# Optimization experiments

Measured on AMD Instinct MI355X. Metric: run time of the kernel, lower is better.

The kernel has to match this reference:

```python
import jax, jax.numpy as jnp
import numpy as np

N_NODES = 100000
N_EDGES = 3200000
D_IN = 128
HEADS = 8
F_OUT = 64


def setup_inputs() -> dict:
    key = jax.random.key(0)
    k1, k2, k3, k4, k5, k6 = jax.random.split(key, 6)
    node_features = jax.random.normal(k1, (N_NODES, D_IN), dtype=jnp.float32)
    linear_proj = jax.random.normal(k2, (D_IN, HEADS * F_OUT), dtype=jnp.float32) * (1.0 / np.sqrt(D_IN))
    scoring_fn_source = jax.random.normal(k3, (1, HEADS, F_OUT), dtype=jnp.float32) * 0.1
    scoring_fn_target = jax.random.normal(k4, (1, HEADS, F_OUT), dtype=jnp.float32) * 0.1
    edge_index = jax.random.randint(k5, (2, N_EDGES), 0, N_NODES, dtype=jnp.int64)
    return {
        'node_features': node_features,
        'linear_proj': linear_proj,
        'scoring_fn_source': scoring_fn_source,
        'scoring_fn_target': scoring_fn_target,
        'edge_index': edge_index,
    }


def reference(node_features, linear_proj, scoring_fn_source, scoring_fn_target, edge_index):
    # node_features: [N, D_in]; edge_index: [2, E] (row 0 = src, row 1 = trg)
    N = node_features.shape[0]
    H, F = scoring_fn_source.shape[1], scoring_fn_source.shape[2]

    # linear projection: [N, H, F]
    proj = (node_features @ linear_proj).reshape(N, H, F)

    # per-node attention scores: [N, H]
    scores_source = jnp.sum(proj * scoring_fn_source, axis=-1)
    scores_target = jnp.sum(proj * scoring_fn_target, axis=-1)

    src, trg = edge_index[0], edge_index[1]
    # lift to edges + LeakyReLU: [E, H]
    scores_per_edge = jax.nn.leaky_relu(scores_source[src] + scores_target[trg],
                                        negative_slope=0.2)

    # neighborhood-aware softmax over edges sharing the same target node
    seg_max = jax.ops.segment_max(scores_per_edge, trg, num_segments=N)   # [N, H]
    exp_scores = jnp.exp(scores_per_edge - seg_max[trg])                  # [E, H]
    seg_sum = jax.ops.segment_sum(exp_scores, trg, num_segments=N)        # [N, H]
    attentions_per_edge = exp_scores / (seg_sum[trg] + 1e-16)             # [E, H]
    return attentions_per_edge
```

## Files before the change

### kernel.cpp

```cpp
#include <hip/hip_runtime.h>
#include <hip/hip_fp16.h>

#define D_IN   128
#define HEADS  8
#define FOUT   64
#define NOUT   16
#define NPB    128
#define NB_MAX 1024
#define CHUNK  4096
#define NBLK_MAX 1024
#define TPN    8
#define SROWS  64
#define SPAD   129

typedef unsigned __attribute__((ext_vector_type(2))) uint2v;
typedef float    __attribute__((ext_vector_type(4))) float4v;

__device__ __forceinline__ unsigned pack2(float a, float b) {
    union { __half2 h; unsigned u; } c;
    c.h = __floats2half2_rn(a, b);
    return c.u;
}
__device__ __forceinline__ float2 up2(unsigned u) {
    union { unsigned x; __half2 h; } c;
    c.x = u;
    return __half22float2(c.h);
}

__device__ __forceinline__ unsigned ntl_u(const unsigned* p) {
    return __builtin_nontemporal_load(p);
}
__device__ __forceinline__ uint2v ntl_u2(const unsigned* p) {
    return __builtin_nontemporal_load((const uint2v*)p);
}
__device__ __forceinline__ float4v ntl_f4(const float* p) {
    return __builtin_nontemporal_load((const float4v*)p);
}
__device__ __forceinline__ void nts_f4(float* p, float4v v) {
    __builtin_nontemporal_store(v, (float4v*)p);
}

__global__ void k_detect(const unsigned int* __restrict__ idx_w, int nwords,
                         unsigned int* __restrict__ flag) {
    unsigned int local = 0;
    int stride = gridDim.x * blockDim.x;
    for (int i = blockIdx.x * blockDim.x + threadIdx.x; 2 * i + 1 < nwords; i += stride)
        local |= idx_w[2 * i + 1];
    if (__any(local != 0) && (threadIdx.x & 63) == 0)
        atomicOr(flag, 1u);
}

__device__ __forceinline__ void load_edge(const unsigned int* idx, int e, int E,
                                          bool is64, unsigned int& s, unsigned int& t) {
    if (is64) {
        uint2v a = ntl_u2(idx + 2 * (size_t)e);
        uint2v b = ntl_u2(idx + 2 * ((size_t)E + e));
        s = a.x; t = b.x;
    } else {
        s = ntl_u(idx + e);
        t = ntl_u(idx + (size_t)E + e);
    }
}

__device__ __forceinline__ unsigned int load_trg(const unsigned int* idx, int e, int E,
                                                 bool is64) {
    if (is64) { uint2v b = ntl_u2(idx + 2 * ((size_t)E + e)); return b.x; }
    return ntl_u(idx + (size_t)E + e);
}

__global__ void k_fold_w(const float* __restrict__ W,
                         const float* __restrict__ a_src,
                         const float* __restrict__ a_trg,
                         float* __restrict__ Wc,
                         unsigned int* __restrict__ flag) {
    int t = blockIdx.x * blockDim.x + threadIdx.x;
    if (t == 0) *flag = 0u;
    if (t >= D_IN * HEADS) return;
    int d = t >> 3, h = t & 7;
    const float* wrow = W + d * (HEADS * FOUT) + h * FOUT;
    float s1 = 0.f, s2 = 0.f;
    #pragma unroll 4
    for (int f = 0; f < FOUT; ++f) {
        float w = wrow[f];
        s1 += w * a_src[h * FOUT + f];
        s2 += w * a_trg[h * FOUT + f];
    }
    Wc[h * D_IN + d]           = s1;
    Wc[(HEADS + h) * D_IN + d] = s2;
}

__global__ void k_scores_t(const float* __restrict__ x,
                           const float* __restrict__ Wc,
                           float* __restrict__ ssrc_f,
                           float* __restrict__ strg_f,
                           __half* __restrict__ ssrc_h, int N) {
    __shared__ float xt[SROWS * SPAD];
    int node0 = blockIdx.x * SROWS;
    int tid   = threadIdx.x;
    int nrows = min(SROWS, N - node0);

    for (int i = tid; i < nrows * 32; i += 256) {
        int r = i >> 5, c = (i & 31) * 4;
        float4v v = ntl_f4(x + (size_t)(node0 + r) * D_IN + c);
        float* dst = &xt[r * SPAD + c];
        dst[0] = v.x; dst[1] = v.y; dst[2] = v.z; dst[3] = v.w;
    }
    __syncthreads();

    int r  = tid & 63;
    int og = tid >> 6;
    if (r >= nrows) return;
    int n = node0 + r;

    const float* w = Wc + og * 4 * D_IN;
    float a0 = 0.f, a1 = 0.f, a2 = 0.f, a3 = 0.f;
    const float* xr = &xt[r * SPAD];
    #pragma unroll 8
    for (int d = 0; d < D_IN; ++d) {
        float xv = xr[d];
        a0 += xv * w[d];
        a1 += xv * w[D_IN + d];
        a2 += xv * w[2 * D_IN + d];
        a3 += xv * w[3 * D_IN + d];
    }

    float4 res = make_float4(a0, a1, a2, a3);
    if (og < 2) *(float4*)(ssrc_f + (size_t)n * HEADS + og * 4)       = res;
    else        *(float4*)(strg_f + (size_t)n * HEADS + (og - 2) * 4) = res;
    if (og < 2) {
        uint2 hp;
        hp.x = pack2(a0, a1);
        hp.y = pack2(a2, a3);
        *(uint2*)(ssrc_h + (size_t)n * HEADS + og * 4) = hp;
    }
}

__global__ void k_hist(const unsigned int* __restrict__ idx, int E,
                       const unsigned int* __restrict__ flag,
                       int* __restrict__ histB, int NB, int NBLK) {
    __shared__ int h[NB_MAX];
    for (int i = threadIdx.x; i < NB; i += blockDim.x) h[i] = 0;
    __syncthreads();
    bool is64 = (*flag == 0u);
    int base = blockIdx.x * CHUNK;
    int lim  = min(base + CHUNK, E);
    for (int e = base + threadIdx.x; e < lim; e += blockDim.x) {
        unsigned int t = load_trg(idx, e, E, is64);
        atomicAdd(&h[t >> 7], 1);
    }
    __syncthreads();
    for (int i = threadIdx.x; i < NB; i += blockDim.x)
        histB[(size_t)i * NBLK + blockIdx.x] = h[i];
}

__global__ void k_scan_blocks(const int* __restrict__ histB,
                              int* __restrict__ histA, int NB, int NBLK,
                              int* __restrict__ binTotal) {
    int b = blockIdx.x;
    __shared__ int v[NBLK_MAX];
    int tid = threadIdx.x;
    v[tid] = (tid < NBLK) ? histB[(size_t)b * NBLK + tid] : 0;
    __syncthreads();
    for (int off = 1; off < NBLK_MAX; off <<= 1) {
        int t = (tid >= off) ? v[tid - off] : 0;
        __syncthreads();
        v[tid] += t;
        __syncthreads();
    }
    if (tid < NBLK)
        histA[(size_t)tid * NB + b] = tid ? v[tid - 1] : 0;
    if (tid == 0)
        binTotal[b] = v[NBLK_MAX - 1];
}

__global__ void k_scan_bins(const int* __restrict__ binTotal, int NB,
                            int* __restrict__ binBase) {
    __shared__ int v[NB_MAX];
    int tid = threadIdx.x;
    v[tid] = (tid < NB) ? binTotal[tid] : 0;
    __syncthreads();
    for (int off = 1; off < NB_MAX; off <<= 1) {
        int t = (tid >= off) ? v[tid - off] : 0;
        __syncthreads();
        v[tid] += t;
        __syncthreads();
    }
    if (tid < NB)
        binBase[tid] = tid ? v[tid - 1] : 0;
}

__global__ void k_scatter(const unsigned int* __restrict__ idx, int E,
                          const unsigned int* __restrict__ flag,
                          const int* __restrict__ histA, int NB,
                          const int* __restrict__ binBase,
                          unsigned int* __restrict__ binned) {
    __shared__ int cnt[NB_MAX];
    for (int i = threadIdx.x; i < NB; i += blockDim.x)
        cnt[i] = binBase[i] + histA[(size_t)blockIdx.x * NB + i];
    __syncthreads();
    bool is64 = (*flag == 0u);
    int base = blockIdx.x * CHUNK;
    int lim  = min(base + CHUNK, E);
    for (int e = base + threadIdx.x; e < lim; e += blockDim.x) {
        unsigned int s, t;
        load_edge(idx, e, E, is64, s, t);
        int pos = atomicAdd(&cnt[t >> 7], 1);
        binned[pos] = s | ((t & 127u) << 20);
    }
}

__global__ void k_sort2(const unsigned int* __restrict__ binned,
                        const int* __restrict__ binBase,
                        const int* __restrict__ binTotal,
                        unsigned int* __restrict__ sortedSrc,
                        int* __restrict__ rowPtr, int N, int NB) {
    __shared__ int cnt[NPB];
    __shared__ int scn[NPB];
    int b = blockIdx.x;
    int node0 = b << 7;
    int start = binBase[b], total = binTotal[b];
    int i = threadIdx.x;

    if (i < NPB) cnt[i] = 0;
    __syncthreads();
    for (int e = i; e < total; e += blockDim.x)
        atomicAdd(&cnt[binned[start + e] >> 20], 1);
    __syncthreads();

    if (i < NPB) scn[i] = cnt[i];
    __syncthreads();
    for (int off = 1; off < NPB; off <<= 1) {
        int t = (i < NPB && i >= off) ? scn[i - off] : 0;
        __syncthreads();
        if (i < NPB) scn[i] += t;
        __syncthreads();
    }
    if (i < NPB) {
        int excl = scn[i] - cnt[i];
        cnt[i] = excl;
        int n = node0 + i;
        if (n < N) rowPtr[n] = start + excl;
    }
    if (b == NB - 1 && i == 0) rowPtr[N] = start + total;
    __syncthreads();

    for (int e = i; e < total; e += blockDim.x) {
        unsigned int v = binned[start + e];
        int pos = atomicAdd(&cnt[v >> 20], 1);
        sortedSrc[start + pos] = v & 0xFFFFFu;
    }
}

__global__ void k_nodesum(const unsigned int* __restrict__ sortedSrc,
                          const int* __restrict__ rowPtr,
                          const __half* __restrict__ ssrc_h,
                          const float* __restrict__ strg_f,
                          __half* __restrict__ combo, int N) {
    int gt = blockIdx.x * blockDim.x + threadIdx.x;
    int n  = gt >> 3;
    int k  = gt & (TPN - 1);
    if (n >= N) return;

    int r0 = rowPtr[n], r1 = rowPtr[n + 1];
    const float4* tp = (const float4*)(strg_f + (size_t)n * HEADS);
    float4 ta = tp[0], tb = tp[1];
    float st[8] = { ta.x, ta.y, ta.z, ta.w, tb.x, tb.y, tb.z, tb.w };
    float acc[8] = { 0, 0, 0, 0, 0, 0, 0, 0 };

    for (int e = r0 + k; e < r1; e += TPN) {
        unsigned int s = sortedSrc[e];
        uint4 sv = *(const uint4*)(ssrc_h + (size_t)s * HEADS);
        float2 f01 = up2(sv.x), f23 = up2(sv.y), f45 = up2(sv.z), f67 = up2(sv.w);
        float vs[8] = { f01.x, f01.y, f23.x, f23.y, f45.x, f45.y, f67.x, f67.y };
        #pragma unroll
        for (int h = 0; h < HEADS; ++h) {
            float sc = vs[h] + st[h];
            sc = sc > 0.f ? sc : 0.2f * sc;
            acc[h] += expf(sc);
        }
    }
    #pragma unroll
    for (int h = 0; h < HEADS; ++h) {
        acc[h] += __shfl_xor(acc[h], 1, 64);
        acc[h] += __shfl_xor(acc[h], 2, 64);
        acc[h] += __shfl_xor(acc[h], 4, 64);
    }
    if (k == 0) {
        float rs[8];
        #pragma unroll
        for (int h = 0; h < HEADS; ++h) rs[h] = 1.0f / (acc[h] + 1e-16f);
        uint4 c0, c1;
        c0.x = pack2(st[0], st[1]);  c0.y = pack2(st[2], st[3]);
        c0.z = pack2(st[4], st[5]);  c0.w = pack2(st[6], st[7]);
        c1.x = pack2(rs[0], rs[1]);  c1.y = pack2(rs[2], rs[3]);
        c1.z = pack2(rs[4], rs[5]);  c1.w = pack2(rs[6], rs[7]);
        uint4* cp = (uint4*)(combo + (size_t)n * 16);
        cp[0] = c0;
        cp[1] = c1;
    }
}

__global__ void k_edge_out_c(const unsigned int* __restrict__ idx, int E,
                             const __half* __restrict__ ssrc_h,
                             const __half* __restrict__ combo,
                             const unsigned int* __restrict__ flag,
                             float* __restrict__ out) {
    int e = blockIdx.x * blockDim.x + threadIdx.x;
    if (e >= E) return;
    bool is64 = (*flag == 0u);
    unsigned int s, t;
    load_edge(idx, e, E, is64, s, t);

    uint4 sv = *(const uint4*)(ssrc_h + (size_t)s * HEADS);
    const uint4* cp = (const uint4*)(combo + (size_t)t * 16);
    uint4 c0 = cp[0], c1 = cp[1];

    float2 s01 = up2(sv.x), s23 = up2(sv.y), s45 = up2(sv.z), s67 = up2(sv.w);
    float2 t01 = up2(c0.x), t23 = up2(c0.y), t45 = up2(c0.z), t67 = up2(c0.w);
    float2 r01 = up2(c1.x), r23 = up2(c1.y), r45 = up2(c1.z), r67 = up2(c1.w);

    float ss[8] = { s01.x, s01.y, s23.x, s23.y, s45.x, s45.y, s67.x, s67.y };
    float st[8] = { t01.x, t01.y, t23.x, t23.y, t45.x, t45.y, t67.x, t67.y };
    float rs[8] = { r01.x, r01.y, r23.x, r23.y, r45.x, r45.y, r67.x, r67.y };

    float o[8];
    #pragma unroll
    for (int h = 0; h < HEADS; ++h) {
        float sc = ss[h] + st[h];
        sc = sc > 0.f ? sc : 0.2f * sc;
        o[h] = expf(sc) * rs[h];
    }
    float4v o0 = { o[0], o[1], o[2], o[3] };
    float4v o1 = { o[4], o[5], o[6], o[7] };
    nts_f4(out + (size_t)e * HEADS,     o0);
    nts_f4(out + (size_t)e * HEADS + 4, o1);
}

__device__ __forceinline__ void edge_scores(const float* ssrc, const float* strg,
                                            unsigned int s, unsigned int t, float* ex) {
    const float4* sp = (const float4*)(ssrc + (size_t)s * HEADS);
    const float4* tp = (const float4*)(strg + (size_t)t * HEADS);
    float4 sa = sp[0], sb = sp[1], ta = tp[0], tb = tp[1];
    float v[8] = { sa.x + ta.x, sa.y + ta.y, sa.z + ta.z, sa.w + ta.w,
                   sb.x + tb.x, sb.y + tb.y, sb.z + tb.z, sb.w + tb.w };
    #pragma unroll
    for (int h = 0; h < HEADS; ++h) {
        float sc = v[h];
        sc = sc > 0.f ? sc : 0.2f * sc;
        ex[h] = expf(sc);
    }
}

__global__ void k_edge_sum(const unsigned int* __restrict__ idx, int E,
                           const float* __restrict__ ssrc,
                           const float* __restrict__ strg,
                           float* __restrict__ sums,
                           const unsigned int* __restrict__ flag) {
    int e = blockIdx.x * blockDim.x + threadIdx.x;
    if (e >= E) return;
    bool is64 = (*flag == 0u);
    unsigned int s, t;
    load_edge(idx, e, E, is64, s, t);
    float ex[8];
    edge_scores(ssrc, strg, s, t, ex);
    float* dst = sums + (size_t)t * HEADS;
    #pragma unroll
    for (int h = 0; h < HEADS; ++h)
        atomicAdd(dst + h, ex[h]);
}

__global__ void k_edge_out(const unsigned int* __restrict__ idx, int E,
                           const float* __restrict__ ssrc,
                           const float* __restrict__ strg,
                           const float* __restrict__ sums,
                           const unsigned int* __restrict__ flag,
                           float* __restrict__ out) {
    int e = blockIdx.x * blockDim.x + threadIdx.x;
    if (e >= E) return;
    bool is64 = (*flag == 0u);
    unsigned int s, t;
    load_edge(idx, e, E, is64, s, t);
    float ex[8];
    edge_scores(ssrc, strg, s, t, ex);
    const float4* sm = (const float4*)(sums + (size_t)t * HEADS);
    float4 m0 = sm[0], m1 = sm[1];
    float4 o0, o1;
    o0.x = ex[0] / (m0.x + 1e-16f);  o0.y = ex[1] / (m0.y + 1e-16f);
    o0.z = ex[2] / (m0.z + 1e-16f);  o0.w = ex[3] / (m0.w + 1e-16f);
    o1.x = ex[4] / (m1.x + 1e-16f);  o1.y = ex[5] / (m1.y + 1e-16f);
    o1.z = ex[6] / (m1.z + 1e-16f);  o1.w = ex[7] / (m1.w + 1e-16f);
    float4* op = (float4*)(out + (size_t)e * HEADS);
    op[0] = o0;
    op[1] = o1;
}

extern "C" void kernel_launch(void* const* d_in, const int* in_sizes, int n_in,
                              void* d_out, int out_size, void* d_ws, size_t ws_size,
                              hipStream_t stream) {
    const float*        x     = (const float*)d_in[0];
    const float*        W     = (const float*)d_in[1];
    const float*        a_src = (const float*)d_in[2];
    const float*        a_trg = (const float*)d_in[3];
    const unsigned int* idx   = (const unsigned int*)d_in[4];

    const int N  = in_sizes[0] / D_IN;
    const int E  = in_sizes[4] / 2;
    const int NH = N * HEADS;
    const int NB   = (N + NPB - 1) / NPB;
    const int NBLK = (E + CHUNK - 1) / CHUNK;

    float* out = (float*)d_out;

    char*  ws  = (char*)d_ws;
    size_t off = 0;
    auto alloc = [&](size_t bytes) { size_t o = off; off = (off + bytes + 255) & ~(size_t)255; return o; };
    size_t NHb = (size_t)NH * sizeof(float);
    float*        sums     = (float*)(ws + alloc(NHb));
    unsigned int* flag     = (unsigned int*)(ws + alloc(4));
    float*        ssrc_f   = (float*)(ws + alloc(NHb));
    float*        strg_f   = (float*)(ws + alloc(NHb));
    __half*       ssrc_h   = (__half*)(ws + alloc((size_t)NH * sizeof(__half)));
    __half*       combo    = (__half*)(ws + alloc((size_t)N * 16 * sizeof(__half)));
    float*        Wc       = (float*)(ws + alloc(NOUT * D_IN * sizeof(float)));
    int*          histA    = (int*)(ws + alloc((size_t)NBLK * NB * sizeof(int)));
    int*          histB    = (int*)(ws + alloc((size_t)NB * NBLK * sizeof(int)));
    int*          binTotal = (int*)(ws + alloc((size_t)NB * sizeof(int)));
    int*          binBase  = (int*)(ws + alloc((size_t)NB * sizeof(int)));
    unsigned int* binned   = (unsigned int*)(ws + alloc((size_t)E * sizeof(unsigned int)));
    unsigned int* sortedS  = (unsigned int*)(ws + alloc((size_t)E * sizeof(unsigned int)));
    int*          rowPtr   = (int*)(ws + alloc((size_t)(N + 1) * sizeof(int)));

    const bool fast = (off <= ws_size) && (NB <= NB_MAX) && (NBLK <= NBLK_MAX)
                      && (N < (1 << 20));

    if (!fast)
        hipMemsetAsync(sums, 0, NHb, stream);

    k_fold_w <<<(D_IN * HEADS + 255) / 256, 256, 0, stream>>>(W, a_src, a_trg, Wc, flag);

    int dwords = in_sizes[4];
    if (dwords > (1 << 20)) dwords = 1 << 20;
    k_detect <<<128, 256, 0, stream>>>(idx, dwords, flag);

    k_scores_t <<<(N + SROWS - 1) / SROWS, 256, 0, stream>>>(x, Wc, ssrc_f, strg_f,
                                                             ssrc_h, N);

    int eblocks = (E + 255) / 256;
    if (fast) {
        k_hist        <<<NBLK, 512, 0, stream>>>(idx, E, flag, histB, NB, NBLK);
        k_scan_blocks <<<NB, NBLK_MAX, 0, stream>>>(histB, histA, NB, NBLK, binTotal);
        k_scan_bins   <<<1, NB_MAX, 0, stream>>>(binTotal, NB, binBase);
        k_scatter     <<<NBLK, 512, 0, stream>>>(idx, E, flag, histA, NB, binBase, binned);
        k_sort2       <<<NB, 512, 0, stream>>>(binned, binBase, binTotal, sortedS,
                                               rowPtr, N, NB);
        k_nodesum     <<<(N * TPN + 511) / 512, 512, 0, stream>>>(sortedS, rowPtr,
                                                                  ssrc_h, strg_f,
                                                                  combo, N);
        k_edge_out_c  <<<eblocks, 256, 0, stream>>>(idx, E, ssrc_h, combo, flag, out);
    } else {
        k_edge_sum <<<eblocks, 256, 0, stream>>>(idx, E, ssrc_f, strg_f, sums, flag);
        k_edge_out <<<eblocks, 256, 0, stream>>>(idx, E, ssrc_f, strg_f, sums, flag, out);
    }
}
```

Measured before the change: 261.4 us.

## Fuse sort with node sums, merge scans, fold detect into score kernel

Fuses the per-bin counting sort with the per-node exp-sum reduction so the sorted sources are consumed in the same block, which removes the rowPtr array and a separate launch. Bin totals are now accumulated with atomics in the histogram kernel, so the two scan kernels merge into one launch. Index-width detection moves into the first blocks of the score kernel. Bin size grows to 512 nodes and chunk size to 8192 edges, which cuts launch count and the size of the histogram scan, at the cost of fewer, larger sort blocks with more shared-memory atomic contention.

```diff
diff --git a/kernel.cpp b/kernel.cpp
--- a/kernel.cpp
+++ b/kernel.cpp
@@ -5,13 +5,15 @@
 #define HEADS  8
 #define FOUT   64
 #define NOUT   16
-#define NPB    128
+#define NPB    512
+#define NPB_SH 9
 #define NB_MAX 1024
-#define CHUNK  4096
+#define CHUNK  8192
 #define NBLK_MAX 1024
 #define TPN    8
 #define SROWS  64
 #define SPAD   129
+#define DET_BLOCKS 128
 
 typedef unsigned __attribute__((ext_vector_type(2))) uint2v;
 typedef float    __attribute__((ext_vector_type(4))) float4v;
@@ -38,16 +40,6 @@
 }
 __device__ __forceinline__ void nts_f4(float* p, float4v v) {
     __builtin_nontemporal_store(v, (float4v*)p);
-}
-
-__global__ void k_detect(const unsigned int* __restrict__ idx_w, int nwords,
-                         unsigned int* __restrict__ flag) {
-    unsigned int local = 0;
-    int stride = gridDim.x * blockDim.x;
-    for (int i = blockIdx.x * blockDim.x + threadIdx.x; 2 * i + 1 < nwords; i += stride)
-        local |= idx_w[2 * i + 1];
-    if (__any(local != 0) && (threadIdx.x & 63) == 0)
-        atomicOr(flag, 1u);
 }
 
 __device__ __forceinline__ void load_edge(const unsigned int* idx, int e, int E,
@@ -72,9 +64,11 @@
                          const float* __restrict__ a_src,
                          const float* __restrict__ a_trg,
                          float* __restrict__ Wc,
-                         unsigned int* __restrict__ flag) {
+                         unsigned int* __restrict__ flag,
+                         int* __restrict__ binTotal, int NB) {
     int t = blockIdx.x * blockDim.x + threadIdx.x;
     if (t == 0) *flag = 0u;
+    if (t < NB) binTotal[t] = 0;
     if (t >= D_IN * HEADS) return;
     int d = t >> 3, h = t & 7;
     const float* wrow = W + d * (HEADS * FOUT) + h * FOUT;
@@ -93,7 +87,18 @@
                            const float* __restrict__ Wc,
                            float* __restrict__ ssrc_f,
                            float* __restrict__ strg_f,
-                           __half* __restrict__ ssrc_h, int N) {
+                           __half* __restrict__ ssrc_h, int N,
+                           const unsigned int* __restrict__ idx_w, int dwords,
+                           unsigned int* __restrict__ flag) {
+    if (blockIdx.x < DET_BLOCKS) {
+        unsigned int local = 0;
+        int stride = DET_BLOCKS * 256;
+        for (int i = blockIdx.x * 256 + threadIdx.x; 2 * i + 1 < dwords; i += stride)
+            local |= idx_w[2 * i + 1];
+        if (__any(local != 0) && (threadIdx.x & 63) == 0)
+            atomicOr(flag, 1u);
+    }
+
     __shared__ float xt[SROWS * SPAD];
     int node0 = blockIdx.x * SROWS;
     int tid   = threadIdx.x;
@@ -137,7 +142,8 @@
 
 __global__ void k_hist(const unsigned int* __restrict__ idx, int E,
                        const unsigned int* __restrict__ flag,
-                       int* __restrict__ histB, int NB, int NBLK) {
+                       int* __restrict__ histB, int NB, int NBLK,
+                       int* __restrict__ binTotal) {
     __shared__ int h[NB_MAX];
     for (int i = threadIdx.x; i < NB; i += blockDim.x) h[i] = 0;
     __syncthreads();
@@ -146,47 +152,46 @@
     int lim  = min(base + CHUNK, E);
     for (int e = base + threadIdx.x; e < lim; e += blockDim.x) {
         unsigned int t = load_trg(idx, e, E, is64);
-        atomicAdd(&h[t >> 7], 1);
-    }
-    __syncthreads();
-    for (int i = threadIdx.x; i < NB; i += blockDim.x)
+        atomicAdd(&h[t >> NPB_SH], 1);
+    }
+    __syncthreads();
+    for (int i = threadIdx.x; i < NB; i += blockDim.x) {
         histB[(size_t)i * NBLK + blockIdx.x] = h[i];
-}
-
-__global__ void k_scan_blocks(const int* __restrict__ histB,
-                              int* __restrict__ histA, int NB, int NBLK,
-                              int* __restrict__ binTotal) {
+        if (h[i]) atomicAdd(&binTotal[i], h[i]);
+    }
+}
+
+__global__ void k_scan(const int* __restrict__ histB,
+                       int* __restrict__ histA, int NB, int NBLK,
+                       const int* __restrict__ binTotal,
+                       int* __restrict__ binBase) {
     int b = blockIdx.x;
-    __shared__ int v[NBLK_MAX];
     int tid = threadIdx.x;
-    v[tid] = (tid < NBLK) ? histB[(size_t)b * NBLK + tid] : 0;
-    __syncthreads();
-    for (int off = 1; off < NBLK_MAX; off <<= 1) {
-        int t = (tid >= off) ? v[tid - off] : 0;
+    if (b < NB) {
+        __shared__ int v[NBLK_MAX];
+        v[tid] = (tid < NBLK) ? histB[(size_t)b * NBLK + tid] : 0;
         __syncthreads();
-        v[tid] += t;
+        for (int off = 1; off < NBLK_MAX; off <<= 1) {
+            int t = (tid >= off) ? v[tid - off] : 0;
+            __syncthreads();
+            v[tid] += t;
+            __syncthreads();
+        }
+        if (tid < NBLK)
+            histA[(size_t)tid * NB + b] = tid ? v[tid - 1] : 0;
+    } else {
+        __shared__ int v[NB_MAX];
+        v[tid] = (tid < NB) ? binTotal[tid] : 0;
         __syncthreads();
-    }
-    if (tid < NBLK)
-        histA[(size_t)tid * NB + b] = tid ? v[tid - 1] : 0;
-    if (tid == 0)
-        binTotal[b] = v[NBLK_MAX - 1];
-}
-
-__global__ void k_scan_bins(const int* __restrict__ binTotal, int NB,
-                            int* __restrict__ binBase) {
-    __shared__ int v[NB_MAX];
-    int tid = threadIdx.x;
-    v[tid] = (tid < NB) ? binTotal[tid] : 0;
-    __syncthreads();
-    for (int off = 1; off < NB_MAX; off <<= 1) {
-        int t = (tid >= off) ? v[tid - off] : 0;
-        __syncthreads();
-        v[tid] += t;
-        __syncthreads();
-    }
-    if (tid < NB)
-        binBase[tid] = tid ? v[tid - 1] : 0;
+        for (int off = 1; off < NB_MAX; off <<= 1) {
+            int t = (tid >= off) ? v[tid - off] : 0;
+            __syncthreads();
+            v[tid] += t;
+            __syncthreads();
+        }
+        if (tid < NB)
+            binBase[tid] = tid ? v[tid - 1] : 0;
+    }
 }
 
 __global__ void k_scatter(const unsigned int* __restrict__ idx, int E,
@@ -204,99 +209,96 @@
     for (int e = base + threadIdx.x; e < lim; e += blockDim.x) {
         unsigned int s, t;
         load_edge(idx, e, E, is64, s, t);
-        int pos = atomicAdd(&cnt[t >> 7], 1);
-        binned[pos] = s | ((t & 127u) << 20);
-    }
-}
-
-__global__ void k_sort2(const unsigned int* __restrict__ binned,
-                        const int* __restrict__ binBase,
-                        const int* __restrict__ binTotal,
-                        unsigned int* __restrict__ sortedSrc,
-                        int* __restrict__ rowPtr, int N, int NB) {
+        int pos = atomicAdd(&cnt[t >> NPB_SH], 1);
+        binned[pos] = s | ((t & (NPB - 1u)) << 20);
+    }
+}
+
+__global__ void k_sortsum(const unsigned int* __restrict__ binned,
+                          const int* __restrict__ binBase,
+                          const int* __restrict__ binTotal,
+                          const __half* __restrict__ ssrc_h,
+                          const float* __restrict__ strg_f,
+                          unsigned int* __restrict__ sortedSrc,
+                          __half* __restrict__ combo, int N, int NB) {
     __shared__ int cnt[NPB];
     __shared__ int scn[NPB];
+    __shared__ int off[NPB];
     int b = blockIdx.x;
-    int node0 = b << 7;
+    int node0 = b << NPB_SH;
     int start = binBase[b], total = binTotal[b];
     int i = threadIdx.x;
 
-    if (i < NPB) cnt[i] = 0;
-    __syncthreads();
-    for (int e = i; e < total; e += blockDim.x)
+    cnt[i] = 0;
+    __syncthreads();
+    for (int e = i; e < total; e += NPB)
         atomicAdd(&cnt[binned[start + e] >> 20], 1);
     __syncthreads();
 
-    if (i < NPB) scn[i] = cnt[i];
-    __syncthreads();
-    for (int off = 1; off < NPB; off <<= 1) {
-        int t = (i < NPB && i >= off) ? scn[i - off] : 0;
+    scn[i] = cnt[i];
+    __syncthreads();
+    for (int o = 1; o < NPB; o <<= 1) {
+        int t = (i >= o) ? scn[i - o] : 0;
         __syncthreads();
-        if (i < NPB) scn[i] += t;
+        scn[i] += t;
         __syncthreads();
     }
-    if (i < NPB) {
-        int excl = scn[i] - cnt[i];
-        cnt[i] = excl;
-        int n = node0 + i;
-        if (n < N) rowPtr[n] = start + excl;
-    }
-    if (b == NB - 1 && i == 0) rowPtr[N] = start + total;
-    __syncthreads();
-
-    for (int e = i; e < total; e += blockDim.x) {
+    off[i] = scn[i] - cnt[i];
+    cnt[i] = off[i];
+    __syncthreads();
+
+    for (int e = i; e < total; e += NPB) {
         unsigned int v = binned[start + e];
         int pos = atomicAdd(&cnt[v >> 20], 1);
         sortedSrc[start + pos] = v & 0xFFFFFu;
     }
-}
-
-__global__ void k_nodesum(const unsigned int* __restrict__ sortedSrc,
-                          const int* __restrict__ rowPtr,
-                          const __half* __restrict__ ssrc_h,
-                          const float* __restrict__ strg_f,
-                          __half* __restrict__ combo, int N) {
-    int gt = blockIdx.x * blockDim.x + threadIdx.x;
-    int n  = gt >> 3;
-    int k  = gt & (TPN - 1);
-    if (n >= N) return;
-
-    int r0 = rowPtr[n], r1 = rowPtr[n + 1];
-    const float4* tp = (const float4*)(strg_f + (size_t)n * HEADS);
-    float4 ta = tp[0], tb = tp[1];
-    float st[8] = { ta.x, ta.y, ta.z, ta.w, tb.x, tb.y, tb.z, tb.w };
-    float acc[8] = { 0, 0, 0, 0, 0, 0, 0, 0 };
-
-    for (int e = r0 + k; e < r1; e += TPN) {
-        unsigned int s = sortedSrc[e];
-        uint4 sv = *(const uint4*)(ssrc_h + (size_t)s * HEADS);
-        float2 f01 = up2(sv.x), f23 = up2(sv.y), f45 = up2(sv.z), f67 = up2(sv.w);
-        float vs[8] = { f01.x, f01.y, f23.x, f23.y, f45.x, f45.y, f67.x, f67.y };
+    __threadfence_block();
+    __syncthreads();
+
+    int k  = i & (TPN - 1);
+    int lg = i >> 3;
+    for (int l = lg; l < NPB; l += NPB / TPN) {
+        int n = node0 + l;
+        if (n >= N) break;
+        int r0 = start + off[l];
+        int r1 = start + scn[l];
+
+        const float4* tp = (const float4*)(strg_f + (size_t)n * HEADS);
+        float4 ta = tp[0], tb = tp[1];
+        float st[8] = { ta.x, ta.y, ta.z, ta.w, tb.x, tb.y, tb.z, tb.w };
+        float acc[8] = { 0, 0, 0, 0, 0, 0, 0, 0 };
+
+        for (int e = r0 + k; e < r1; e += TPN) {
+            unsigned int s = sortedSrc[e];
+            uint4 sv = *(const uint4*)(ssrc_h + (size_t)s * HEADS);
+            float2 f01 = up2(sv.x), f23 = up2(sv.y), f45 = up2(sv.z), f67 = up2(sv.w);
+            float vs[8] = { f01.x, f01.y, f23.x, f23.y, f45.x, f45.y, f67.x, f67.y };
+            #pragma unroll
+            for (int h = 0; h < HEADS; ++h) {
+                float sc = vs[h] + st[h];
+                sc = sc > 0.f ? sc : 0.2f * sc;
+                acc[h] += expf(sc);
+            }
+        }
         #pragma unroll
         for (int h = 0; h < HEADS; ++h) {
-            float sc = vs[h] + st[h];
-            sc = sc > 0.f ? sc : 0.2f * sc;
-            acc[h] += expf(sc);
+            acc[h] += __shfl_xor(acc[h], 1, 64);
+            acc[h] += __shfl_xor(acc[h], 2, 64);
+            acc[h] += __shfl_xor(acc[h], 4, 64);
         }
-    }
-    #pragma unroll
-    for (int h = 0; h < HEADS; ++h) {
-        acc[h] += __shfl_xor(acc[h], 1, 64);
-        acc[h] += __shfl_xor(acc[h], 2, 64);
-        acc[h] += __shfl_xor(acc[h], 4, 64);
-    }
-    if (k == 0) {
-        float rs[8];
-        #pragma unroll
-        for (int h = 0; h < HEADS; ++h) rs[h] = 1.0f / (acc[h] + 1e-16f);
-        uint4 c0, c1;
-        c0.x = pack2(st[0], st[1]);  c0.y = pack2(st[2], st[3]);
-        c0.z = pack2(st[4], st[5]);  c0.w = pack2(st[6], st[7]);
-        c1.x = pack2(rs[0], rs[1]);  c1.y = pack2(rs[2], rs[3]);
-        c1.z = pack2(rs[4], rs[5]);  c1.w = pack2(rs[6], rs[7]);
-        uint4* cp = (uint4*)(combo + (size_t)n * 16);
-        cp[0] = c0;
-        cp[1] = c1;
+        if (k == 0) {
+            float rs[8];
+            #pragma unroll
+            for (int h = 0; h < HEADS; ++h) rs[h] = 1.0f / (acc[h] + 1e-16f);
+            uint4 c0, c1;
+            c0.x = pack2(st[0], st[1]);  c0.y = pack2(st[2], st[3]);
+            c0.z = pack2(st[4], st[5]);  c0.w = pack2(st[6], st[7]);
+            c1.x = pack2(rs[0], rs[1]);  c1.y = pack2(rs[2], rs[3]);
+            c1.z = pack2(rs[4], rs[5]);  c1.w = pack2(rs[6], rs[7]);
+            uint4* cp = (uint4*)(combo + (size_t)n * 16);
+            cp[0] = c0;
+            cp[1] = c1;
+        }
     }
 }
 
@@ -349,6 +351,16 @@
         sc = sc > 0.f ? sc : 0.2f * sc;
         ex[h] = expf(sc);
     }
+}
+
+__global__ void k_detect_fb(const unsigned int* __restrict__ idx_w, int nwords,
+                            unsigned int* __restrict__ flag) {
+    unsigned int local = 0;
+    int stride = gridDim.x * blockDim.x;
+    for (int i = blockIdx.x * blockDim.x + threadIdx.x; 2 * i + 1 < nwords; i += stride)
+        local |= idx_w[2 * i + 1];
+    if (__any(local != 0) && (threadIdx.x & 63) == 0)
+        atomicOr(flag, 1u);
 }
 
 __global__ void k_edge_sum(const unsigned int* __restrict__ idx, int E,
@@ -428,36 +440,35 @@
     int*          binBase  = (int*)(ws + alloc((size_t)NB * sizeof(int)));
     unsigned int* binned   = (unsigned int*)(ws + alloc((size_t)E * sizeof(unsigned int)));
     unsigned int* sortedS  = (unsigned int*)(ws + alloc((size_t)E * sizeof(unsigned int)));
-    int*          rowPtr   = (int*)(ws + alloc((size_t)(N + 1) * sizeof(int)));
 
     const bool fast = (off <= ws_size) && (NB <= NB_MAX) && (NBLK <= NBLK_MAX)
                       && (N < (1 << 20));
 
-    if (!fast)
-        hipMemsetAsync(sums, 0, NHb, stream);
-
-    k_fold_w <<<(D_IN * HEADS + 255) / 256, 256, 0, stream>>>(W, a_src, a_trg, Wc, flag);
-
     int dwords = in_sizes[4];
     if (dwords > (1 << 20)) dwords = 1 << 20;
-    k_detect <<<128, 256, 0, stream>>>(idx, dwords, flag);
-
-    k_scores_t <<<(N + SROWS - 1) / SROWS, 256, 0, stream>>>(x, Wc, ssrc_f, strg_f,
-                                                             ssrc_h, N);
-
-    int eblocks = (E + 255) / 256;
+
+    k_fold_w <<<(D_IN * HEADS + 255) / 256, 256, 0, stream>>>(W, a_src, a_trg, Wc,
+                                                              flag, binTotal, NB);
+
     if (fast) {
-        k_hist        <<<NBLK, 512, 0, stream>>>(idx, E, flag, histB, NB, NBLK);
-        k_scan_blocks <<<NB, NBLK_MAX, 0, stream>>>(histB, histA, NB, NBLK, binTotal);
-        k_scan_bins   <<<1, NB_MAX, 0, stream>>>(binTotal, NB, binBase);
-        k_scatter     <<<NBLK, 512, 0, stream>>>(idx, E, flag, histA, NB, binBase, binned);
-        k_sort2       <<<NB, 512, 0, stream>>>(binned, binBase, binTotal, sortedS,
-                                               rowPtr, N, NB);
-        k_nodesum     <<<(N * TPN + 511) / 512, 512, 0, stream>>>(sortedS, rowPtr,
-                                                                  ssrc_h, strg_f,
-                                                                  combo, N);
-        k_edge_out_c  <<<eblocks, 256, 0, stream>>>(idx, E, ssrc_h, combo, flag, out);
+        k_scores_t <<<(N + SROWS - 1) / SROWS, 256, 0, stream>>>(x, Wc, ssrc_f, strg_f,
+                                                                 ssrc_h, N,
+                                                                 idx, dwords, flag);
+        k_hist    <<<NBLK, 512, 0, stream>>>(idx, E, flag, histB, NB, NBLK, binTotal);
+        k_scan    <<<NB + 1, NBLK_MAX, 0, stream>>>(histB, histA, NB, NBLK,
+                                                    binTotal, binBase);
+        k_scatter <<<NBLK, 512, 0, stream>>>(idx, E, flag, histA, NB, binBase, binned);
+        k_sortsum <<<NB, NPB, 0, stream>>>(binned, binBase, binTotal, ssrc_h, strg_f,
+                                           sortedS, combo, N, NB);
+        k_edge_out_c <<<(E + 255) / 256, 256, 0, stream>>>(idx, E, ssrc_h, combo,
+                                                           flag, out);
     } else {
+        hipMemsetAsync(sums, 0, NHb, stream);
+        k_detect_fb <<<128, 256, 0, stream>>>(idx, dwords, flag);
+        k_scores_t <<<(N + SROWS - 1) / SROWS, 256, 0, stream>>>(x, Wc, ssrc_f, strg_f,
+                                                                 ssrc_h, N,
+                                                                 idx, 0, flag);
+        int eblocks = (E + 255) / 256;
         k_edge_sum <<<eblocks, 256, 0, stream>>>(idx, E, ssrc_f, strg_f, sums, flag);
         k_edge_out <<<eblocks, 256, 0, stream>>>(idx, E, ssrc_f, strg_f, sums, flag, out);
     }
```

After: 238.9 us. 8.6% less time.
